# Performance work log

Measured on AMD Instinct MI355X. Metric: run time of the kernel, lower is better.

The kernel has to match this reference:

```python
import jax, jax.numpy as jnp
import numpy as np
import math

C = 512
EPS = 1e-5


def _ln(x, g, b):
    m = jnp.mean(x, axis=-1, keepdims=True)
    v = jnp.var(x, axis=-1, keepdims=True)
    return (x - m) * jax.lax.rsqrt(v + EPS) * g + b


def _attn(x, w_qkv, w_out):
    # x: (..., L, C); attention over axis -2 (axial)
    qkv = jnp.einsum('...lc,dc->...ld', x, w_qkv)          # (..., L, 3C)
    qkv = qkv.reshape(*qkv.shape[:-1], C, 3)               # interleaved split as in torch reshape(*shape,3)
    q, k, v = qkv[..., 0], qkv[..., 1], qkv[..., 2]
    scale = 1.0 / math.sqrt(C)
    logits = jnp.einsum('...qc,...kc->...qk', q, k) * scale
    p = jax.nn.softmax(logits, axis=-1)
    ctx = jnp.einsum('...qk,...kc->...qc', p, v)
    return jnp.einsum('...lc,dc->...ld', ctx, w_out)


def setup_inputs() -> dict:
    key = jax.random.key(0)
    ks = jax.random.split(key, 16)
    s = 0.02
    inp = {
        'x': jax.random.normal(ks[0], (8, C, 48, 192), jnp.float32),
        'w_qkv1': jax.random.normal(ks[1], (3 * C, C), jnp.float32) * s,
        'w_out1': jax.random.normal(ks[2], (C, C), jnp.float32) * s,
        'w_qkv2': jax.random.normal(ks[3], (3 * C, C), jnp.float32) * s,
        'w_out2': jax.random.normal(ks[4], (C, C), jnp.float32) * s,
        'g1': jnp.ones((C,), jnp.float32), 'b1': jnp.zeros((C,), jnp.float32),
        'g2': jnp.ones((C,), jnp.float32), 'b2': jnp.zeros((C,), jnp.float32),
        'g3': jnp.ones((C,), jnp.float32), 'b3': jnp.zeros((C,), jnp.float32),
        'w_fc1': jax.random.normal(ks[5], (4 * C, C), jnp.float32) * s,
        'b_fc1': jnp.zeros((4 * C,), jnp.float32),
        'w_fc2': jax.random.normal(ks[6], (C, 4 * C), jnp.float32) * s,
        'b_fc2': jnp.zeros((C,), jnp.float32),
    }
    return inp


def reference(x, w_qkv1, w_out1, w_qkv2, w_out2, g1, b1, g2, b2, g3, b3,
              w_fc1, b_fc1, w_fc2, b_fc2):
    # x: (B, C, H, W) -> (B, W, H, C)
    x = jnp.transpose(x, (0, 3, 2, 1))
    x = x + _attn(_ln(x, g1, b1), w_qkv1, w_out1)          # attention along H
    # (B, W, H, C) -> (B, H, W, C)
    x = jnp.transpose(x, (0, 2, 1, 3))
    x = x + _attn(_ln(x, g2, b2), w_qkv2, w_out2)          # attention along W
    h = _ln(x, g3, b3)
    h = jax.nn.relu(jnp.einsum('bhwc,dc->bhwd', h, w_fc1) + b_fc1)
    x = x + jnp.einsum('bhwd,cd->bhwc', h, w_fc2) + b_fc2
    # (B, H, W, C) -> (B, C, H, W)
    return jnp.transpose(x, (0, 3, 1, 2))
```

## Files before the change

### kernel.cpp

```cpp
#include <hip/hip_runtime.h>

typedef unsigned short u16;
typedef __attribute__((ext_vector_type(8))) short short8;
typedef __attribute__((ext_vector_type(8))) __bf16 bf16x8;
typedef __attribute__((ext_vector_type(4))) float f32x4;

#define DEV __device__ __forceinline__

DEV u16 f2bf(float f){ unsigned u = __float_as_uint(f); return (u16)((u + 0x7fffu + ((u>>16)&1u)) >> 16); }
DEV float bf2f(u16 h){ return __uint_as_float(((unsigned)h)<<16); }

DEV f32x4 mfma_bf16(short8 a, short8 b, f32x4 c){
  return __builtin_amdgcn_mfma_f32_16x16x32_bf16(
      __builtin_bit_cast(bf16x8, a), __builtin_bit_cast(bf16x8, b), c, 0, 0, 0);
}

DEV void gl2lds16(const u16* g, u16* s){
  __builtin_amdgcn_global_load_lds(
      (__attribute__((address_space(1))) void*)(g),
      (__attribute__((address_space(3))) void*)(s), 16, 0, 0);
}

#define BB 8
#define HH 48
#define WW 192
#define CC 512
#define NTOK (BB*HH*WW)

__global__ void k_permqkv(const float* __restrict__ w, u16* __restrict__ o){
  int i = blockIdx.x*256 + threadIdx.x;
  int n = i >> 9, kk = i & 511;
  int src = 3*(n & 511) + (n >> 9);
  o[i] = f2bf(w[src*512 + kk]);
}
__global__ void k_conv(const float* __restrict__ w, u16* __restrict__ o, int nelem){
  int i = blockIdx.x*256 + threadIdx.x;
  if (i < nelem) o[i] = f2bf(w[i]);
}

__global__ void k_tin(const float* __restrict__ x, float* __restrict__ xr){
  __shared__ float T[32][33];
  int bh = blockIdx.x / 96, rem = blockIdx.x % 96;
  int c0 = (rem/6)*32, w0 = (rem%6)*32;
  int b = bh / HH, h = bh % HH;
  const float* xp = x + ((size_t)b*CC*HH + h)*WW;
  #pragma unroll
  for (int p=0;p<4;p++){
    int idx = p*256 + threadIdx.x;
    int cc = idx >> 5, ww = idx & 31;
    T[cc][ww] = xp[(size_t)(c0+cc)*(HH*WW) + w0 + ww];
  }
  __syncthreads();
  float* xo = xr + (size_t)bh*WW*CC;
  #pragma unroll
  for (int p=0;p<4;p++){
    int idx = p*256 + threadIdx.x;
    int ww = idx >> 5, cc = idx & 31;
    xo[(size_t)(w0+ww)*CC + c0 + cc] = T[cc][ww];
  }
}

__global__ void k_tout(const float* __restrict__ xr, float* __restrict__ out){
  __shared__ float T[32][33];
  int bh = blockIdx.x / 96, rem = blockIdx.x % 96;
  int c0 = (rem/6)*32, w0 = (rem%6)*32;
  int b = bh / HH, h = bh % HH;
  const float* xi = xr + (size_t)bh*WW*CC;
  #pragma unroll
  for (int p=0;p<4;p++){
    int idx = p*256 + threadIdx.x;
    int ww = idx >> 5, cc = idx & 31;
    T[ww][cc] = xi[(size_t)(w0+ww)*CC + c0 + cc];
  }
  __syncthreads();
  float* op = out + ((size_t)b*CC*HH + h)*WW;
  #pragma unroll
  for (int p=0;p<4;p++){
    int idx = p*256 + threadIdx.x;
    int cc = idx >> 5, ww = idx & 31;
    op[(size_t)(c0+cc)*(HH*WW) + w0 + ww] = T[ww][cc];
  }
}

__global__ void k_ln(const float* __restrict__ xr, const float* __restrict__ g,
                     const float* __restrict__ bb, u16* __restrict__ y){
  int t = blockIdx.x*4 + (threadIdx.x>>6);
  int lane = threadIdx.x & 63;
  const float* row = xr + (size_t)t*CC + lane*8;
  float v[8];
  *(f32x4*)(v)   = *(const f32x4*)(row);
  *(f32x4*)(v+4) = *(const f32x4*)(row+4);
  float s=0.f, s2=0.f;
  #pragma unroll
  for (int j=0;j<8;j++){ s += v[j]; s2 += v[j]*v[j]; }
  #pragma unroll
  for (int o=32;o;o>>=1){ s += __shfl_xor(s,o); s2 += __shfl_xor(s2,o); }
  float mean = s*(1.f/CC);
  float var  = s2*(1.f/CC) - mean*mean;
  float rs = rsqrtf(var + 1e-5f);
  const float* gp = g + lane*8; const float* bp = bb + lane*8;
  short8 o8;
  #pragma unroll
  for (int j=0;j<8;j++) o8[j] = (short)f2bf((v[j]-mean)*rs*gp[j] + bp[j]);
  *(short8*)(y + (size_t)t*CC + lane*8) = o8;
}

__global__ __launch_bounds__(256)
void k_gemm(const u16* __restrict__ A, int lda,
            const u16* __restrict__ Bw, int ldb,
            void* __restrict__ Out, int ldo,
            const float* __restrict__ bias,
            int K, int nbn, int epi){
  __shared__ __align__(16) u16 As[128*64];
  __shared__ __align__(16) u16 Bs[128*64];
  int mb = blockIdx.x / nbn, nb = blockIdx.x % nbn;
  int tid = threadIdx.x, lane = tid & 63, wv = tid >> 6;
  size_t m0 = (size_t)mb*128, n0 = (size_t)nb*128;
  int lr = lane >> 3;
  int cc0 = (lane & 7) ^ lr;
  const u16* gA = A  + (m0 + wv*32 + lr)*(size_t)lda + cc0*8;
  const u16* gB = Bw + (n0 + wv*32 + lr)*(size_t)ldb + cc0*8;
  u16* sA = As + wv*32*64;
  u16* sB = Bs + wv*32*64;
  int m = lane & 15, quad = lane >> 4;
  int wm = (wv>>1)*64, wn = (wv&1)*64;
  int off0 = ((quad    ) ^ (m & 7))*8;
  int off1 = ((quad + 4) ^ (m & 7))*8;
  f32x4 acc[4][4];
  #pragma unroll
  for (int i=0;i<4;i++)
    #pragma unroll
    for (int j=0;j<4;j++) acc[i][j] = (f32x4){0.f,0.f,0.f,0.f};
  const u16* aB = As + (wm + m)*64;
  const u16* bB = Bs + (wn + m)*64;
  for (int k0 = 0; k0 < K; k0 += 64){
    #pragma unroll
    for (int t=0;t<4;t++){
      gl2lds16(gA + (size_t)(t*8)*lda, sA + t*8*64);
      gl2lds16(gB + (size_t)(t*8)*ldb, sB + t*8*64);
    }
    gA += 64; gB += 64;
    __syncthreads();
    {
      short8 af[4], bf[4];
      #pragma unroll
      for (int i=0;i<4;i++) af[i] = *(const short8*)(aB + i*16*64 + off0);
      #pragma unroll
      for (int j=0;j<4;j++) bf[j] = *(const short8*)(bB + j*16*64 + off0);
      #pragma unroll
      for (int i=0;i<4;i++)
        #pragma unroll
        for (int j=0;j<4;j++)
          acc[i][j] = mfma_bf16(af[i], bf[j], acc[i][j]);
    }
    {
      short8 af[4], bf[4];
      #pragma unroll
      for (int i=0;i<4;i++) af[i] = *(const short8*)(aB + i*16*64 + off1);
      #pragma unroll
      for (int j=0;j<4;j++) bf[j] = *(const short8*)(bB + j*16*64 + off1);
      #pragma unroll
      for (int i=0;i<4;i++)
        #pragma unroll
        for (int j=0;j<4;j++)
          acc[i][j] = mfma_bf16(af[i], bf[j], acc[i][j]);
    }
    __syncthreads();
  }
  if (epi == 2){
    float* O = (float*)Out + (m0 + wm + quad*4)*(size_t)ldo + n0 + wn + m;
    #pragma unroll
    for (int j=0;j<4;j++){
      float bv = bias ? bias[n0 + wn + j*16 + m] : 0.f;
      #pragma unroll
      for (int i=0;i<4;i++)
        #pragma unroll
        for (int r=0;r<4;r++)
          O[(size_t)(i*16+r)*ldo + j*16] += acc[i][j][r] + bv;
    }
  } else {
    u16* O = (u16*)Out + (m0 + wm + quad*4)*(size_t)ldo + n0 + wn + m;
    #pragma unroll
    for (int j=0;j<4;j++){
      float bv = bias ? bias[n0 + wn + j*16 + m] : 0.f;
      #pragma unroll
      for (int i=0;i<4;i++)
        #pragma unroll
        for (int r=0;r<4;r++){
          float v = acc[i][j][r] + bv;
          if (epi == 1) v = fmaxf(v, 0.f);
          O[(size_t)(i*16+r)*ldo + j*16] = f2bf(v);
        }
    }
  }
}

__global__ void k_qk(const u16* __restrict__ q, const u16* __restrict__ kp, int ldq,
                     float* __restrict__ S, int L, int nt,
                     int SD, int OUTs, int INN, int LST, float scale){
  int blk = blockIdx.x;
  int s = blk / (nt*nt), tl = blk % (nt*nt);
  int ti = tl / nt, tj = tl % nt;
  int lane = threadIdx.x, m = lane & 15, quad = lane >> 4;
  size_t tokbase = (size_t)(s/SD)*OUTs + (size_t)(s%SD)*INN;
  const u16* qr = q  + (tokbase + (size_t)(ti*16+m)*LST)*ldq + quad*8;
  const u16* kr = kp + (tokbase + (size_t)(tj*16+m)*LST)*ldq + quad*8;
  f32x4 acc = (f32x4){0.f,0.f,0.f,0.f};
  #pragma unroll
  for (int kk=0; kk<CC; kk+=32)
    acc = mfma_bf16(*(const short8*)(qr+kk), *(const short8*)(kr+kk), acc);
  float* Sp = S + (size_t)s*L*L + (size_t)(ti*16 + quad*4)*L + tj*16 + m;
  #pragma unroll
  for (int r=0;r<4;r++) Sp[(size_t)r*L] = acc[r]*scale;
}

__global__ void k_softmax(const float* __restrict__ S, u16* __restrict__ P, int L, int Lp){
  int row = blockIdx.x*4 + (threadIdx.x>>6);
  int lane = threadIdx.x & 63;
  const float* sr = S + (size_t)row*L;
  float v0 = (lane      < L) ? sr[lane]      : -3.0e38f;
  float v1 = (lane+64   < L) ? sr[lane+64]   : -3.0e38f;
  float v2 = (lane+128  < L) ? sr[lane+128]  : -3.0e38f;
  float mx = fmaxf(v0, fmaxf(v1, v2));
  #pragma unroll
  for (int o=32;o;o>>=1) mx = fmaxf(mx, __shfl_xor(mx, o));
  float e0 = (lane      < L) ? __expf(v0-mx) : 0.f;
  float e1 = (lane+64   < L) ? __expf(v1-mx) : 0.f;
  float e2 = (lane+128  < L) ? __expf(v2-mx) : 0.f;
  float sm = e0+e1+e2;
  #pragma unroll
  for (int o=32;o;o>>=1) sm += __shfl_xor(sm, o);
  float inv = 1.f/sm;
  u16* pr = P + (size_t)row*Lp;
  if (lane      < Lp) pr[lane]      = f2bf(e0*inv);
  if (lane+64   < Lp) pr[lane+64]   = f2bf(e1*inv);
  if (lane+128  < Lp) pr[lane+128]  = f2bf(e2*inv);
}

__global__ void k_vt(const u16* __restrict__ v, int ldv, u16* __restrict__ vt,
                     int L, int Lp, int SD, int OUTs, int INN, int LST){
  __shared__ float T[32*193];
  int s = blockIdx.x >> 4;
  int c0 = (blockIdx.x & 15)*32;
  size_t tokbase = (size_t)(s/SD)*OUTs + (size_t)(s%SD)*INN;
  int pad = Lp + 1;
  for (int idx = threadIdx.x; idx < L*32; idx += 256){
    int l = idx >> 5, cc = idx & 31;
    T[cc*pad + l] = bf2f(v[(tokbase + (size_t)l*LST)*ldv + c0 + cc]);
  }
  __syncthreads();
  u16* vo = vt + ((size_t)s*CC + c0)*Lp;
  for (int idx = threadIdx.x; idx < 32*Lp; idx += 256){
    int cc = idx / Lp, l = idx - cc*Lp;
    vo[idx] = (l < L) ? f2bf(T[cc*pad + l]) : (u16)0;
  }
}

template<int L, int Lp, int NTQ, int NCJ>
__global__ __launch_bounds__(256)
void k_pv2(const u16* __restrict__ P, const u16* __restrict__ vt, u16* __restrict__ ctx,
           int SD, int OUTs, int INN, int LST){
  constexpr int G   = 32 / NCJ;
  constexpr int LPP = Lp + 8;
  constexpr int CW  = NCJ * 16;
  constexpr int CJW = NCJ / 4;
  constexpr int NKS = Lp / 32;
  constexpr int SHW = (L*LPP > L*CW) ? L*LPP : L*CW;
  __shared__ __align__(16) u16 SH[SHW];

  int sq = blockIdx.x / G, g = blockIdx.x % G;
  int tid = threadIdx.x, lane = tid & 63, wv = tid >> 6;
  int m = lane & 15, quad = lane >> 4;

  const u16* Pg = P + (size_t)sq * L * Lp;
  constexpr int PU = L * Lp / 8;
  for (int u = tid; u < PU; u += 256){
    int r = u / (Lp/8), c = u % (Lp/8);
    *(short8*)(SH + r*LPP + c*8) = *(const short8*)(Pg + (size_t)r*Lp + c*8);
  }
  __syncthreads();

  short8 bfr[CJW][NKS];
  #pragma unroll
  for (int lc = 0; lc < CJW; lc++){
    const u16* vr = vt + ((size_t)sq*CC + (size_t)((g*NCJ + (wv*CJW + lc))*16 + m))*Lp + quad*8;
    #pragma unroll
    for (int ks = 0; ks < NKS; ks++) bfr[lc][ks] = *(const short8*)(vr + ks*32);
  }

  f32x4 acc[CJW][NTQ];
  #pragma unroll
  for (int lc = 0; lc < CJW; lc++)
    #pragma unroll
    for (int qt = 0; qt < NTQ; qt++) acc[lc][qt] = (f32x4){0.f,0.f,0.f,0.f};

  #pragma unroll
  for (int qt = 0; qt < NTQ; qt++){
    short8 a[NKS];
    #pragma unroll
    for (int ks = 0; ks < NKS; ks++)
      a[ks] = *(const short8*)(SH + (qt*16 + m)*LPP + quad*8 + ks*32);
    #pragma unroll
    for (int lc = 0; lc < CJW; lc++)
      #pragma unroll
      for (int ks = 0; ks < NKS; ks++)
        acc[lc][qt] = mfma_bf16(a[ks], bfr[lc][ks], acc[lc][qt]);
  }
  __syncthreads();

  #pragma unroll
  for (int qt = 0; qt < NTQ; qt++)
    #pragma unroll
    for (int lc = 0; lc < CJW; lc++)
      #pragma unroll
      for (int r = 0; r < 4; r++)
        SH[(qt*16 + quad*4 + r)*CW + (wv*CJW + lc)*16 + m] = f2bf(acc[lc][qt][r]);
  __syncthreads();

  size_t tokbase = (size_t)(sq/SD)*OUTs + (size_t)(sq%SD)*INN;
  constexpr int CU8 = CW / 8;
  constexpr int TU = L * CU8;
  for (int u = tid; u < TU; u += 256){
    int l = u / CU8, c = u % CU8;
    *(short8*)(ctx + (tokbase + (size_t)l*LST)*CC + g*CW + c*8) =
        *(const short8*)(SH + l*CW + c*8);
  }
}

extern "C" void kernel_launch(void* const* d_in, const int* in_sizes, int n_in,
                              void* d_out, int out_size, void* d_ws, size_t ws_size,
                              hipStream_t stream){
  const float* x      = (const float*)d_in[0];
  const float* wqkv1  = (const float*)d_in[1];
  const float* wout1  = (const float*)d_in[2];
  const float* wqkv2  = (const float*)d_in[3];
  const float* wout2  = (const float*)d_in[4];
  const float* g1 = (const float*)d_in[5];  const float* b1 = (const float*)d_in[6];
  const float* g2 = (const float*)d_in[7];  const float* b2 = (const float*)d_in[8];
  const float* g3 = (const float*)d_in[9];  const float* b3 = (const float*)d_in[10];
  const float* wfc1 = (const float*)d_in[11]; const float* bfc1 = (const float*)d_in[12];
  const float* wfc2 = (const float*)d_in[13]; const float* bfc2 = (const float*)d_in[14];

  char* ws = (char*)d_ws;
  size_t off = 0;
  auto alloc = [&](size_t bytes)->char*{
    char* p = ws + off; off += (bytes + 255) & ~(size_t)255; return p;
  };
  float* xres = (float*)alloc((size_t)NTOK*CC*4);
  u16*   y    = (u16*)  alloc((size_t)NTOK*CC*2);
  u16*   qkv  = (u16*)  alloc((size_t)NTOK*1536*2);
  u16* wqkv1p = (u16*)alloc((size_t)1536*512*2);
  u16* wqkv2p = (u16*)alloc((size_t)1536*512*2);
  u16* wout1p = (u16*)alloc((size_t)512*512*2);
  u16* wout2p = (u16*)alloc((size_t)512*512*2);
  u16* wfc1p  = (u16*)alloc((size_t)2048*512*2);
  u16* wfc2p  = (u16*)alloc((size_t)512*2048*2);
  u16*   hv   = qkv;

  u16*   P    = (u16*)d_out;
  u16*   vt   = (u16*)((char*)d_out + 28311552);
  float* S    = (float*)((char*)d_out + 28311552);
  (void)ws_size; (void)in_sizes; (void)n_in; (void)out_size;

  const float scale = 0.044194173824159216f;

  k_permqkv<<<3072, 256, 0, stream>>>(wqkv1, wqkv1p);
  k_permqkv<<<3072, 256, 0, stream>>>(wqkv2, wqkv2p);
  k_conv<<<1024, 256, 0, stream>>>(wout1, wout1p, 512*512);
  k_conv<<<1024, 256, 0, stream>>>(wout2, wout2p, 512*512);
  k_conv<<<4096, 256, 0, stream>>>(wfc1, wfc1p, 2048*512);
  k_conv<<<4096, 256, 0, stream>>>(wfc2, wfc2p, 512*2048);

  k_tin<<<BB*HH*96, 256, 0, stream>>>(x, xres);

  k_ln<<<NTOK/4, 256, 0, stream>>>(xres, g1, b1, y);
  k_gemm<<<576*12, 256, 0, stream>>>(y, 512, wqkv1p, 512, qkv, 1536, nullptr, 512, 12, 0);
  k_qk<<<1536*9, 64, 0, stream>>>(qkv, qkv+512, 1536, S, 48, 3, 192, 9216, 1, 192, scale);
  k_softmax<<<NTOK/4, 256, 0, stream>>>(S, P, 48, 64);
  k_vt<<<1536*16, 256, 0, stream>>>(qkv+1024, 1536, vt, 48, 64, 192, 9216, 1, 192);
  k_pv2<48,64,3,16><<<1536*2, 256, 0, stream>>>(P, vt, y, 192, 9216, 1, 192);
  k_gemm<<<576*4, 256, 0, stream>>>(y, 512, wout1p, 512, xres, 512, nullptr, 512, 4, 2);

  k_ln<<<NTOK/4, 256, 0, stream>>>(xres, g2, b2, y);
  k_gemm<<<576*12, 256, 0, stream>>>(y, 512, wqkv2p, 512, qkv, 1536, nullptr, 512, 12, 0);
  k_qk<<<384*144, 64, 0, stream>>>(qkv, qkv+512, 1536, S, 192, 12, 48, 9216, 192, 1, scale);
  k_softmax<<<NTOK/4, 256, 0, stream>>>(S, P, 192, 192);
  k_vt<<<384*16, 256, 0, stream>>>(qkv+1024, 1536, vt, 192, 192, 48, 9216, 192, 1);
  k_pv2<192,192,12,8><<<384*4, 256, 0, stream>>>(P, vt, y, 48, 9216, 192, 1);
  k_gemm<<<576*4, 256, 0, stream>>>(y, 512, wout2p, 512, xres, 512, nullptr, 512, 4, 2);

  k_ln<<<NTOK/4, 256, 0, stream>>>(xres, g3, b3, y);
  for (int half = 0; half < 2; half++){
    size_t M0 = (size_t)half * 36864;
    k_gemm<<<288*16, 256, 0, stream>>>(y + M0*512, 512, wfc1p, 512, hv, 2048, bfc1, 512, 16, 1);
    k_gemm<<<288*4, 256, 0, stream>>>(hv, 2048, wfc2p, 2048, xres + M0*512, 512, bfc2, 2048, 4, 2);
  }

  k_tout<<<BB*HH*96, 256, 0, stream>>>(xres, (float*)d_out);
}
```

Before: 2.215 ms.

## Replace GEMM with 256x256 tiled, double-buffered, 8-wave pipelined MFMA kernel

Replaces the 128x128 single-buffered GEMM with a 256x256 tile kernel that uses 512 threads (8 waves) and double-buffered LDS. Global-to-LDS loads for the next K-steps are interleaved with MFMA phases, using explicit waitcnt, sched barriers and setprio. The epilogue becomes a template parameter. This is meant to hide load latency and raise data reuse per tile. In exchange it uses 128KB of LDS and more accumulator registers, and it launches fewer blocks, so the small out-projection GEMMs may underfill the GPU.

```diff
diff --git a/kernel.cpp b/kernel.cpp
--- a/kernel.cpp
+++ b/kernel.cpp
@@ -105,90 +105,160 @@
   *(short8*)(y + (size_t)t*CC + lane*8) = o8;
 }
 
-__global__ __launch_bounds__(256)
-void k_gemm(const u16* __restrict__ A, int lda,
-            const u16* __restrict__ Bw, int ldb,
-            void* __restrict__ Out, int ldo,
-            const float* __restrict__ bias,
-            int K, int nbn, int epi){
-  __shared__ __align__(16) u16 As[128*64];
-  __shared__ __align__(16) u16 Bs[128*64];
-  int mb = blockIdx.x / nbn, nb = blockIdx.x % nbn;
-  int tid = threadIdx.x, lane = tid & 63, wv = tid >> 6;
-  size_t m0 = (size_t)mb*128, n0 = (size_t)nb*128;
-  int lr = lane >> 3;
-  int cc0 = (lane & 7) ^ lr;
-  const u16* gA = A  + (m0 + wv*32 + lr)*(size_t)lda + cc0*8;
-  const u16* gB = Bw + (n0 + wv*32 + lr)*(size_t)ldb + cc0*8;
-  u16* sA = As + wv*32*64;
-  u16* sB = Bs + wv*32*64;
-  int m = lane & 15, quad = lane >> 4;
-  int wm = (wv>>1)*64, wn = (wv&1)*64;
-  int off0 = ((quad    ) ^ (m & 7))*8;
-  int off1 = ((quad + 4) ^ (m & 7))*8;
-  f32x4 acc[4][4];
-  #pragma unroll
-  for (int i=0;i<4;i++)
+template<int EPI>
+__global__ __launch_bounds__(512, 2)
+void k_gemm256(const u16* __restrict__ A, int lda,
+               const u16* __restrict__ Bw, int ldb,
+               void* __restrict__ Out, int ldo,
+               const float* __restrict__ bias,
+               int K, int nbn){
+  __shared__ __align__(16) u16 As[2*16384];
+  __shared__ __align__(16) u16 Bs[2*16384];
+  const int tid = threadIdx.x, lane = tid & 63, wv = tid >> 6;
+  const int m = lane & 15, quad = lane >> 4;
+  const int wr = wv >> 2, wc = wv & 3;
+  const int mb = blockIdx.x / nbn, nb = blockIdx.x % nbn;
+  const size_t m0 = (size_t)mb * 256, n0 = (size_t)nb * 256;
+
+  const int srow = wv*8 + (lane >> 3);
+  const int schk = ((lane & 7) ^ (lane >> 3)) * 8;
+  const u16* gA = A  + (m0 + srow) * (size_t)lda + schk;
+  const u16* gB = Bw + (n0 + srow) * (size_t)ldb + schk;
+  const int sdst = wv * 8 * 64;
+  const int NT = K >> 6;
+
+#define STG_A(bufi, tt, p) gl2lds16(gA + (size_t)(p)*64*lda + (size_t)(tt)*64, \
+                                    As + (bufi)*16384 + (p)*4096 + sdst)
+#define STG_B(bufi, tt, p) gl2lds16(gB + (size_t)(p)*64*ldb + (size_t)(tt)*64, \
+                                    Bs + (bufi)*16384 + (p)*4096 + sdst)
+#define WAIT_LGKM0 asm volatile("s_waitcnt lgkmcnt(0)" ::: "memory")
+#define WAIT_VM4   asm volatile("s_waitcnt vmcnt(4)" ::: "memory")
+#define WAIT_VM0   asm volatile("s_waitcnt vmcnt(0)" ::: "memory")
+#define SCHED0 __builtin_amdgcn_sched_barrier(0)
+#define BAR    __builtin_amdgcn_s_barrier()
+#define PRIO1  __builtin_amdgcn_s_setprio(1)
+#define PRIO0  __builtin_amdgcn_s_setprio(0)
+
+  STG_A(0,0,0); STG_A(0,0,1); STG_A(0,0,2); STG_A(0,0,3);
+  STG_B(0,0,0); STG_B(0,0,1); STG_B(0,0,2); STG_B(0,0,3);
+  STG_A(1,1,0); STG_A(1,1,2); STG_A(1,1,1); STG_A(1,1,3);
+
+  f32x4 acc[8][4];
+  #pragma unroll
+  for (int i=0;i<8;i++)
     #pragma unroll
     for (int j=0;j<4;j++) acc[i][j] = (f32x4){0.f,0.f,0.f,0.f};
-  const u16* aB = As + (wm + m)*64;
-  const u16* bB = Bs + (wn + m)*64;
-  for (int k0 = 0; k0 < K; k0 += 64){
-    #pragma unroll
-    for (int t=0;t<4;t++){
-      gl2lds16(gA + (size_t)(t*8)*lda, sA + t*8*64);
-      gl2lds16(gB + (size_t)(t*8)*ldb, sB + t*8*64);
-    }
-    gA += 64; gB += 64;
-    __syncthreads();
-    {
-      short8 af[4], bf[4];
-      #pragma unroll
-      for (int i=0;i<4;i++) af[i] = *(const short8*)(aB + i*16*64 + off0);
-      #pragma unroll
-      for (int j=0;j<4;j++) bf[j] = *(const short8*)(bB + j*16*64 + off0);
-      #pragma unroll
-      for (int i=0;i<4;i++)
-        #pragma unroll
-        for (int j=0;j<4;j++)
-          acc[i][j] = mfma_bf16(af[i], bf[j], acc[i][j]);
-    }
-    {
-      short8 af[4], bf[4];
-      #pragma unroll
-      for (int i=0;i<4;i++) af[i] = *(const short8*)(aB + i*16*64 + off1);
-      #pragma unroll
-      for (int j=0;j<4;j++) bf[j] = *(const short8*)(bB + j*16*64 + off1);
-      #pragma unroll
-      for (int i=0;i<4;i++)
-        #pragma unroll
-        for (int j=0;j<4;j++)
-          acc[i][j] = mfma_bf16(af[i], bf[j], acc[i][j]);
-    }
-    __syncthreads();
-  }
-  if (epi == 2){
-    float* O = (float*)Out + (m0 + wm + quad*4)*(size_t)ldo + n0 + wn + m;
+
+  const int off0 = ( quad      ^ (m & 7)) * 8;
+  const int off1 = ((quad + 4) ^ (m & 7)) * 8;
+
+  WAIT_VM4;
+  BAR;
+
+  for (int t = 0; t < NT; ++t){
+    const int buf = t & 1, obuf = buf ^ 1;
+    const u16* aB = As + buf*16384 + (wr*128 + m)*64;
+    const u16* bB = Bs + buf*16384 + (wc*64  + m)*64;
+    short8 av[4][2], bv[4][2];
+
+    #pragma unroll
+    for (int i=0;i<4;i++){
+      av[i][0] = *(const short8*)(aB + i*1024 + off0);
+      av[i][1] = *(const short8*)(aB + i*1024 + off1);
+    }
+    #pragma unroll
+    for (int j=0;j<2;j++){
+      bv[j][0] = *(const short8*)(bB + j*1024 + off0);
+      bv[j][1] = *(const short8*)(bB + j*1024 + off1);
+    }
+    if (t + 1 < NT){ STG_B(obuf, t+1, 0); STG_B(obuf, t+1, 1); }
+    WAIT_LGKM0; SCHED0;
+    PRIO1;
+    #pragma unroll
+    for (int i=0;i<4;i++)
+      #pragma unroll
+      for (int j=0;j<2;j++){
+        acc[i][j] = mfma_bf16(av[i][0], bv[j][0], acc[i][j]);
+        acc[i][j] = mfma_bf16(av[i][1], bv[j][1], acc[i][j]);
+      }
+    PRIO0;
+
+    #pragma unroll
+    for (int j=0;j<2;j++){
+      bv[2+j][0] = *(const short8*)(bB + (2+j)*1024 + off0);
+      bv[2+j][1] = *(const short8*)(bB + (2+j)*1024 + off1);
+    }
+    if (t + 1 < NT){ STG_B(obuf, t+1, 2); STG_B(obuf, t+1, 3); }
+    WAIT_LGKM0; SCHED0;
+    PRIO1;
+    #pragma unroll
+    for (int i=0;i<4;i++)
+      #pragma unroll
+      for (int j=0;j<2;j++){
+        acc[i][2+j] = mfma_bf16(av[i][0], bv[2+j][0], acc[i][2+j]);
+        acc[i][2+j] = mfma_bf16(av[i][1], bv[2+j][1], acc[i][2+j]);
+      }
+    PRIO0;
+    BAR;
+
+    #pragma unroll
+    for (int i=0;i<4;i++){
+      av[i][0] = *(const short8*)(aB + (i+4)*1024 + off0);
+      av[i][1] = *(const short8*)(aB + (i+4)*1024 + off1);
+    }
+    if (t + 2 < NT){ STG_A(buf, t+2, 0); STG_A(buf, t+2, 2); }
+    WAIT_LGKM0; SCHED0;
+    PRIO1;
+    #pragma unroll
+    for (int i=0;i<4;i++)
+      #pragma unroll
+      for (int j=0;j<2;j++){
+        acc[4+i][2+j] = mfma_bf16(av[i][0], bv[2+j][0], acc[4+i][2+j]);
+        acc[4+i][2+j] = mfma_bf16(av[i][1], bv[2+j][1], acc[4+i][2+j]);
+      }
+    PRIO0;
+    BAR;
+
+    if (t + 2 < NT){ STG_A(buf, t+2, 1); STG_A(buf, t+2, 3); }
+    PRIO1;
+    #pragma unroll
+    for (int i=0;i<4;i++)
+      #pragma unroll
+      for (int j=0;j<2;j++){
+        acc[4+i][j] = mfma_bf16(av[i][0], bv[j][0], acc[4+i][j]);
+        acc[4+i][j] = mfma_bf16(av[i][1], bv[j][1], acc[4+i][j]);
+      }
+    PRIO0;
+    if (t + 2 < NT)      { WAIT_VM4; }
+    else if (t + 1 < NT) { WAIT_VM0; }
+    if (t + 1 < NT) BAR;
+  }
+
+#undef STG_A
+#undef STG_B
+
+  if (EPI == 2){
+    float* O = (float*)Out + (m0 + wr*128 + quad*4)*(size_t)ldo + n0 + wc*64 + m;
     #pragma unroll
     for (int j=0;j<4;j++){
-      float bv = bias ? bias[n0 + wn + j*16 + m] : 0.f;
-      #pragma unroll
-      for (int i=0;i<4;i++)
+      float bvv = bias ? bias[n0 + wc*64 + j*16 + m] : 0.f;
+      #pragma unroll
+      for (int i=0;i<8;i++)
         #pragma unroll
         for (int r=0;r<4;r++)
-          O[(size_t)(i*16+r)*ldo + j*16] += acc[i][j][r] + bv;
+          O[(size_t)(i*16+r)*ldo + j*16] += acc[i][j][r] + bvv;
     }
   } else {
-    u16* O = (u16*)Out + (m0 + wm + quad*4)*(size_t)ldo + n0 + wn + m;
+    u16* O = (u16*)Out + (m0 + wr*128 + quad*4)*(size_t)ldo + n0 + wc*64 + m;
     #pragma unroll
     for (int j=0;j<4;j++){
-      float bv = bias ? bias[n0 + wn + j*16 + m] : 0.f;
-      #pragma unroll
-      for (int i=0;i<4;i++)
+      float bvv = bias ? bias[n0 + wc*64 + j*16 + m] : 0.f;
+      #pragma unroll
+      for (int i=0;i<8;i++)
         #pragma unroll
         for (int r=0;r<4;r++){
-          float v = acc[i][j][r] + bv;
-          if (epi == 1) v = fmaxf(v, 0.f);
+          float v = acc[i][j][r] + bvv;
+          if (EPI == 1) v = fmaxf(v, 0.f);
           O[(size_t)(i*16+r)*ldo + j*16] = f2bf(v);
         }
     }
@@ -374,26 +444,26 @@
   k_tin<<<BB*HH*96, 256, 0, stream>>>(x, xres);
 
   k_ln<<<NTOK/4, 256, 0, stream>>>(xres, g1, b1, y);
-  k_gemm<<<576*12, 256, 0, stream>>>(y, 512, wqkv1p, 512, qkv, 1536, nullptr, 512, 12, 0);
+  k_gemm256<0><<<288*6, 512, 0, stream>>>(y, 512, wqkv1p, 512, qkv, 1536, nullptr, 512, 6);
   k_qk<<<1536*9, 64, 0, stream>>>(qkv, qkv+512, 1536, S, 48, 3, 192, 9216, 1, 192, scale);
   k_softmax<<<NTOK/4, 256, 0, stream>>>(S, P, 48, 64);
   k_vt<<<1536*16, 256, 0, stream>>>(qkv+1024, 1536, vt, 48, 64, 192, 9216, 1, 192);
   k_pv2<48,64,3,16><<<1536*2, 256, 0, stream>>>(P, vt, y, 192, 9216, 1, 192);
-  k_gemm<<<576*4, 256, 0, stream>>>(y, 512, wout1p, 512, xres, 512, nullptr, 512, 4, 2);
+  k_gemm256<2><<<288*2, 512, 0, stream>>>(y, 512, wout1p, 512, xres, 512, nullptr, 512, 2);
 
   k_ln<<<NTOK/4, 256, 0, stream>>>(xres, g2, b2, y);
-  k_gemm<<<576*12, 256, 0, stream>>>(y, 512, wqkv2p, 512, qkv, 1536, nullptr, 512, 12, 0);
+  k_gemm256<0><<<288*6, 512, 0, stream>>>(y, 512, wqkv2p, 512, qkv, 1536, nullptr, 512, 6);
   k_qk<<<384*144, 64, 0, stream>>>(qkv, qkv+512, 1536, S, 192, 12, 48, 9216, 192, 1, scale);
   k_softmax<<<NTOK/4, 256, 0, stream>>>(S, P, 192, 192);
   k_vt<<<384*16, 256, 0, stream>>>(qkv+1024, 1536, vt, 192, 192, 48, 9216, 192, 1);
   k_pv2<192,192,12,8><<<384*4, 256, 0, stream>>>(P, vt, y, 48, 9216, 192, 1);
-  k_gemm<<<576*4, 256, 0, stream>>>(y, 512, wout2p, 512, xres, 512, nullptr, 512, 4, 2);
+  k_gemm256<2><<<288*2, 512, 0, stream>>>(y, 512, wout2p, 512, xres, 512, nullptr, 512, 2);
 
   k_ln<<<NTOK/4, 256, 0, stream>>>(xres, g3, b3, y);
   for (int half = 0; half < 2; half++){
     size_t M0 = (size_t)half * 36864;
-    k_gemm<<<288*16, 256, 0, stream>>>(y + M0*512, 512, wfc1p, 512, hv, 2048, bfc1, 512, 16, 1);
-    k_gemm<<<288*4, 256, 0, stream>>>(hv, 2048, wfc2p, 2048, xres + M0*512, 512, bfc2, 2048, 4, 2);
+    k_gemm256<1><<<144*8, 512, 0, stream>>>(y + M0*512, 512, wfc1p, 512, hv, 2048, bfc1, 512, 8);
+    k_gemm256<2><<<144*2, 512, 0, stream>>>(hv, 2048, wfc2p, 2048, xres + M0*512, 512, bfc2, 2048, 2);
   }
 
   k_tout<<<BB*HH*96, 256, 0, stream>>>(xres, (float*)d_out);
```

Result: slower. 2.468 ms (+11.4%).
